# Kernel optimization log

Hardware: AMD Instinct MI355X
Metric: run time of the kernel (lower is better)

The kernel has to match this reference:

```python
import jax, jax.numpy as jnp
import numpy as np

TAU = 1.0
EPS_NORM = 1e-12  # matches F.normalize default eps
EPS_POS = 1e-5


def setup_inputs() -> dict:
    key = jax.random.key(0)
    kf, kl = jax.random.split(key)
    B, D, NUM_CLASSES = 4096, 128, 1000
    features = jax.random.normal(kf, (B, D), dtype=jnp.float32)
    labels = jax.random.randint(kl, (B,), 0, NUM_CLASSES, dtype=jnp.int64)
    return {"features": features, "labels": labels}


def reference(features, labels):
    B = features.shape[0]
    # cosine similarity via GEMM on L2-normalized features
    norm = jnp.linalg.norm(features, axis=-1, keepdims=True)
    f = features / jnp.maximum(norm, EPS_NORM)
    sim = f @ f.T  # [B, B]
    diag = jnp.eye(B, dtype=bool)
    sim = jnp.where(diag, -jnp.inf, sim)
    # log-softmax over rows at temperature tau; then zero the diagonal
    logp = jax.nn.log_softmax(sim / TAU, axis=-1)
    logp = jnp.where(diag, 0.0, logp)
    # positive-pair mask (same label, excluding self)
    mask = (labels[:, None] == labels[None, :]) & ~diag
    maskf = mask.astype(jnp.float32)
    num_pos = maskf.sum(axis=-1)  # [B]
    pos_sum = (logp * maskf).sum(axis=-1)  # [B]
    loss = -(pos_sum / (num_pos + EPS_POS)).sum() / B
    return loss
```

## Files before the change

### kernel.cpp

```cpp
#include <hip/hip_runtime.h>
#include <math.h>

#define NB 4096
#define ND 128
#define TT 256
#define NT (NB / TT)

typedef __bf16 bf16x8 __attribute__((ext_vector_type(8)));
typedef float  f32x4  __attribute__((ext_vector_type(4)));

__global__ __launch_bounds__(1024) void supcon_mfma(
    const float* __restrict__ f, const int* __restrict__ labels,
    float* __restrict__ partials, float* __restrict__ out)
{
    __shared__ __align__(16) __bf16 At[TT * ND];
    __shared__ __align__(16) __bf16 Bt[TT * ND];
    __shared__ float redL[2][TT][3];

    const int t    = threadIdx.x;
    const int lane = t & 63;
    const int wid  = t >> 6;
    const int wr   = wid >> 1;
    const int wc   = wid & 1;
    const int bi   = blockIdx.x >> 4;
    const int cs   = blockIdx.x & 15;
    const int lr   = lane & 15;
    const int lk   = lane >> 4;
    const int ib   = bi * TT;
    const int jb   = cs * TT;

    if (blockIdx.x == 0 && t == 0) out[0] = 0.f;

    {
        const int c16  = t & 15;
        const int rloc = t >> 4;
        const float* gA = f + (size_t)ib * ND;
        const float* gB = f + (size_t)jb * ND;
#pragma unroll
        for (int s = 0; s < 2; ++s) {
            const float* g = s ? gB : gA;
            __bf16*      T = s ? Bt : At;
#pragma unroll
            for (int p = 0; p < 4; ++p) {
                const int row = p * 64 + rloc;
                const float4 lo = *reinterpret_cast<const float4*>(g + row * ND + c16 * 8);
                const float4 hi = *reinterpret_cast<const float4*>(g + row * ND + c16 * 8 + 4);
                float ss = lo.x*lo.x + lo.y*lo.y + lo.z*lo.z + lo.w*lo.w
                         + hi.x*hi.x + hi.y*hi.y + hi.z*hi.z + hi.w*hi.w;
#pragma unroll
                for (int off = 1; off < 16; off <<= 1) ss += __shfl_xor(ss, off, 64);
                const float inv = 1.0f / fmaxf(sqrtf(ss), 1e-12f);
                bf16x8 o;
                o[0] = (__bf16)(lo.x * inv); o[1] = (__bf16)(lo.y * inv);
                o[2] = (__bf16)(lo.z * inv); o[3] = (__bf16)(lo.w * inv);
                o[4] = (__bf16)(hi.x * inv); o[5] = (__bf16)(hi.y * inv);
                o[6] = (__bf16)(hi.z * inv); o[7] = (__bf16)(hi.w * inv);
                *reinterpret_cast<bf16x8*>(&T[(row * 16 + (c16 ^ (row & 15))) * 8]) = o;
            }
        }
    }

    int ig[2], labi[2];
#pragma unroll
    for (int it = 0; it < 2; ++it) {
        ig[it]   = ib + wr * 32 + it * 16 + lr;
        labi[it] = labels[ig[it]];
    }

    __syncthreads();

    bf16x8 bfr[2][4];
#pragma unroll
    for (int it = 0; it < 2; ++it)
#pragma unroll
        for (int ks = 0; ks < 4; ++ks) {
            const int row = wr * 32 + it * 16 + lr;
            bfr[it][ks] = *reinterpret_cast<const bf16x8*>(
                &At[(row * 16 + ((ks * 4 + lk) ^ lr)) * 8]);
        }

    float es[2] = {}, ps[2] = {}, np[2] = {};

#pragma unroll
    for (int jt = 0; jt < 8; ++jt) {
        bf16x8 af[4];
#pragma unroll
        for (int ks = 0; ks < 4; ++ks) {
            const int row = wc * 128 + jt * 16 + lr;
            af[ks] = *reinterpret_cast<const bf16x8*>(
                &Bt[(row * 16 + ((ks * 4 + lk) ^ lr)) * 8]);
        }
        f32x4 acc[2] = {};
#pragma unroll
        for (int ks = 0; ks < 4; ++ks)
#pragma unroll
            for (int it = 0; it < 2; ++it)
                acc[it] = __builtin_amdgcn_mfma_f32_16x16x32_bf16(
                    af[ks], bfr[it][ks], acc[it], 0, 0, 0);

        const int jg0 = jb + wc * 128 + jt * 16 + lk * 4;
        const int4 lj4 = *reinterpret_cast<const int4*>(&labels[jg0]);
        const int lj[4] = {lj4.x, lj4.y, lj4.z, lj4.w};

#pragma unroll
        for (int it = 0; it < 2; ++it)
#pragma unroll
            for (int r = 0; r < 4; ++r) {
                const int   jgv  = jg0 + r;
                const float s    = acc[it][r];
                const float e    = __expf(s);
                const bool  self = (jgv == ig[it]);
                const bool  pos  = (lj[r] == labi[it]) && !self;
                es[it] += self ? 0.f : e;
                ps[it] += pos ? s : 0.f;
                np[it] += pos ? 1.f : 0.f;
            }
    }

#pragma unroll
    for (int off = 16; off < 64; off <<= 1)
#pragma unroll
        for (int it = 0; it < 2; ++it) {
            es[it] += __shfl_xor(es[it], off, 64);
            ps[it] += __shfl_xor(ps[it], off, 64);
            np[it] += __shfl_xor(np[it], off, 64);
        }
    if (lk == 0) {
#pragma unroll
        for (int it = 0; it < 2; ++it) {
            const int rl = wr * 32 + it * 16 + lr;
            redL[wc][rl][0] = es[it];
            redL[wc][rl][1] = ps[it];
            redL[wc][rl][2] = np[it];
        }
    }
    __syncthreads();
    if (t < TT) {
        float* p = partials + ((size_t)cs * NB + ib + t) * 3;
        p[0] = redL[0][t][0] + redL[1][t][0];
        p[1] = redL[0][t][1] + redL[1][t][1];
        p[2] = redL[0][t][2] + redL[1][t][2];
    }
}

__global__ __launch_bounds__(256) void final_kernel(
    const float* __restrict__ partials, float* __restrict__ out)
{
    const int row = blockIdx.x * 256 + threadIdx.x;
    float es = 0.f, ps = 0.f, np = 0.f;
#pragma unroll
    for (int cs = 0; cs < NT; ++cs) {
        const float* p = partials + ((size_t)cs * NB + row) * 3;
        es += p[0]; ps += p[1]; np += p[2];
    }
    const float lse = logf(es);
    float c = -(ps - np * lse) / ((np + 1e-5f) * (float)NB);
#pragma unroll
    for (int off = 1; off < 64; off <<= 1) c += __shfl_xor(c, off, 64);
    __shared__ float sred[4];
    if ((threadIdx.x & 63) == 0) sred[threadIdx.x >> 6] = c;
    __syncthreads();
    if (threadIdx.x == 0) atomicAdd(out, sred[0] + sred[1] + sred[2] + sred[3]);
}

extern "C" void kernel_launch(void* const* d_in, const int* in_sizes, int n_in,
                              void* d_out, int out_size, void* d_ws, size_t ws_size,
                              hipStream_t stream) {
    const float* features = (const float*)d_in[0];
    const int*   labels   = (const int*)d_in[1];
    float* out = (float*)d_out;
    float* partials = (float*)d_ws;

    supcon_mfma<<<NT * NT, 1024, 0, stream>>>(features, labels, partials, out);
    final_kernel<<<NB / 256, 256, 0, stream>>>(partials, out);
}
```

Measured before the change: 18.73 us.

## Switch similarity GEMM to FP8 MFMA and shrink row tile to 128

Normalized features are packed to FP8 (e4m3) instead of bf16 and fed to the 16x16x32 fp8 MFMA, which halves LDS footprint and fragment traffic. The row tile drops from 256 to 128 with 512-thread blocks, which doubles the grid to 512 blocks for better CU coverage and occupancy. The cost is lower precision in the cosine similarities, which could push the loss outside tolerance. It also means each block reloads and renormalizes the column tile more often.

```diff
diff --git a/kernel.cpp b/kernel.cpp
--- a/kernel.cpp
+++ b/kernel.cpp
@@ -3,19 +3,19 @@
 
 #define NB 4096
 #define ND 128
-#define TT 256
-#define NT (NB / TT)
+#define TI 128
+#define TJ 256
+#define NCS (NB / TJ)
 
-typedef __bf16 bf16x8 __attribute__((ext_vector_type(8)));
-typedef float  f32x4  __attribute__((ext_vector_type(4)));
+typedef float f32x4 __attribute__((ext_vector_type(4)));
 
-__global__ __launch_bounds__(1024) void supcon_mfma(
+__global__ __launch_bounds__(512) void supcon_mfma(
     const float* __restrict__ f, const int* __restrict__ labels,
     float* __restrict__ partials, float* __restrict__ out)
 {
-    __shared__ __align__(16) __bf16 At[TT * ND];
-    __shared__ __align__(16) __bf16 Bt[TT * ND];
-    __shared__ float redL[2][TT][3];
+    __shared__ __align__(16) long At[TI * 16];
+    __shared__ __align__(16) long Bt[TJ * 16];
+    __shared__ float redL[2][TI][3];
 
     const int t    = threadIdx.x;
     const int lane = t & 63;
@@ -26,36 +26,36 @@
     const int cs   = blockIdx.x & 15;
     const int lr   = lane & 15;
     const int lk   = lane >> 4;
-    const int ib   = bi * TT;
-    const int jb   = cs * TT;
+    const int ib   = bi * TI;
+    const int jb   = cs * TJ;
 
     if (blockIdx.x == 0 && t == 0) out[0] = 0.f;
 
     {
-        const int c16  = t & 15;
-        const int rloc = t >> 4;
+        const int c8 = t & 15;
+        const int rl = t >> 4;
         const float* gA = f + (size_t)ib * ND;
         const float* gB = f + (size_t)jb * ND;
 #pragma unroll
         for (int s = 0; s < 2; ++s) {
             const float* g = s ? gB : gA;
-            __bf16*      T = s ? Bt : At;
-#pragma unroll
-            for (int p = 0; p < 4; ++p) {
-                const int row = p * 64 + rloc;
-                const float4 lo = *reinterpret_cast<const float4*>(g + row * ND + c16 * 8);
-                const float4 hi = *reinterpret_cast<const float4*>(g + row * ND + c16 * 8 + 4);
+            long*        T = s ? Bt : At;
+            const int    nr = s ? (TJ / 32) : (TI / 32);
+            for (int p = 0; p < nr; ++p) {
+                const int row = p * 32 + rl;
+                const float4 lo = *reinterpret_cast<const float4*>(g + row * ND + c8 * 8);
+                const float4 hi = *reinterpret_cast<const float4*>(g + row * ND + c8 * 8 + 4);
                 float ss = lo.x*lo.x + lo.y*lo.y + lo.z*lo.z + lo.w*lo.w
                          + hi.x*hi.x + hi.y*hi.y + hi.z*hi.z + hi.w*hi.w;
 #pragma unroll
                 for (int off = 1; off < 16; off <<= 1) ss += __shfl_xor(ss, off, 64);
                 const float inv = 1.0f / fmaxf(sqrtf(ss), 1e-12f);
-                bf16x8 o;
-                o[0] = (__bf16)(lo.x * inv); o[1] = (__bf16)(lo.y * inv);
-                o[2] = (__bf16)(lo.z * inv); o[3] = (__bf16)(lo.w * inv);
-                o[4] = (__bf16)(hi.x * inv); o[5] = (__bf16)(hi.y * inv);
-                o[6] = (__bf16)(hi.z * inv); o[7] = (__bf16)(hi.w * inv);
-                *reinterpret_cast<bf16x8*>(&T[(row * 16 + (c16 ^ (row & 15))) * 8]) = o;
+                int w0 = __builtin_amdgcn_cvt_pk_fp8_f32(lo.x * inv, lo.y * inv, 0, false);
+                w0     = __builtin_amdgcn_cvt_pk_fp8_f32(lo.z * inv, lo.w * inv, w0, true);
+                int w1 = __builtin_amdgcn_cvt_pk_fp8_f32(hi.x * inv, hi.y * inv, 0, false);
+                w1     = __builtin_amdgcn_cvt_pk_fp8_f32(hi.z * inv, hi.w * inv, w1, true);
+                int2 pk; pk.x = w0; pk.y = w1;
+                *reinterpret_cast<int2*>(&T[row * 16 + (c8 ^ (row & 15))]) = pk;
             }
         }
     }
@@ -69,33 +69,31 @@
 
     __syncthreads();
 
-    bf16x8 bfr[2][4];
+    long bfr[2][4];
 #pragma unroll
     for (int it = 0; it < 2; ++it)
 #pragma unroll
         for (int ks = 0; ks < 4; ++ks) {
             const int row = wr * 32 + it * 16 + lr;
-            bfr[it][ks] = *reinterpret_cast<const bf16x8*>(
-                &At[(row * 16 + ((ks * 4 + lk) ^ lr)) * 8]);
+            bfr[it][ks] = At[row * 16 + ((ks * 4 + lk) ^ (row & 15))];
         }
 
     float es[2] = {}, ps[2] = {}, np[2] = {};
 
 #pragma unroll
     for (int jt = 0; jt < 8; ++jt) {
-        bf16x8 af[4];
+        long af[4];
 #pragma unroll
         for (int ks = 0; ks < 4; ++ks) {
             const int row = wc * 128 + jt * 16 + lr;
-            af[ks] = *reinterpret_cast<const bf16x8*>(
-                &Bt[(row * 16 + ((ks * 4 + lk) ^ lr)) * 8]);
+            af[ks] = Bt[row * 16 + ((ks * 4 + lk) ^ (row & 15))];
         }
         f32x4 acc[2] = {};
 #pragma unroll
         for (int ks = 0; ks < 4; ++ks)
 #pragma unroll
             for (int it = 0; it < 2; ++it)
-                acc[it] = __builtin_amdgcn_mfma_f32_16x16x32_bf16(
+                acc[it] = __builtin_amdgcn_mfma_f32_16x16x32_fp8_fp8(
                     af[ks], bfr[it][ks], acc[it], 0, 0, 0);
 
         const int jg0 = jb + wc * 128 + jt * 16 + lk * 4;
@@ -135,7 +133,7 @@
         }
     }
     __syncthreads();
-    if (t < TT) {
+    if (t < TI) {
         float* p = partials + ((size_t)cs * NB + ib + t) * 3;
         p[0] = redL[0][t][0] + redL[1][t][0];
         p[1] = redL[0][t][1] + redL[1][t][1];
@@ -149,7 +147,7 @@
     const int row = blockIdx.x * 256 + threadIdx.x;
     float es = 0.f, ps = 0.f, np = 0.f;
 #pragma unroll
-    for (int cs = 0; cs < NT; ++cs) {
+    for (int cs = 0; cs < NCS; ++cs) {
         const float* p = partials + ((size_t)cs * NB + row) * 3;
         es += p[0]; ps += p[1]; np += p[2];
     }
@@ -171,6 +169,6 @@
     float* out = (float*)d_out;
     float* partials = (float*)d_ws;
 
-    supcon_mfma<<<NT * NT, 1024, 0, stream>>>(features, labels, partials, out);
+    supcon_mfma<<<(NB / TI) * NCS, 512, 0, stream>>>(features, labels, partials, out);
     final_kernel<<<NB / 256, 256, 0, stream>>>(partials, out);
 }
```

Measured after the change: 22.22 us. 18.7% more time.
